# Performance work log

Measured on AMD Instinct MI355X. Metric: run time of the kernel, lower is better.

Reference implementation:

```python
import jax, jax.numpy as jnp
import numpy as np

N = 100000   # nodes
E = 1600000  # directed edges
HID = 64


def gat_conv(x, src, dst, W, a_src, a_dst, b, heads, out_ch):
    """PyG-style GATConv (add_self_loops=True, negative_slope=0.2, concat)."""
    n = x.shape[0]
    h = (x @ W).reshape(n, heads, out_ch)              # [N,H,C]
    loop = jnp.arange(n, dtype=src.dtype)
    s = jnp.concatenate([src, loop])                   # self loops appended
    d = jnp.concatenate([dst, loop])
    alpha_src = jnp.sum(h * a_src, axis=-1)            # [N,H]
    alpha_dst = jnp.sum(h * a_dst, axis=-1)            # [N,H]
    alpha = jax.nn.leaky_relu(alpha_src[s] + alpha_dst[d], 0.2)  # [E+N,H]
    # segment softmax over incoming edges of each destination node
    amax = jax.ops.segment_max(alpha, d, num_segments=n)
    alpha = jnp.exp(alpha - amax[d])
    asum = jax.ops.segment_sum(alpha, d, num_segments=n)
    alpha = alpha / (asum[d] + 1e-16)
    msg = h[s] * alpha[:, :, None]                     # [E+N,H,C]
    out = jax.ops.segment_sum(msg, d, num_segments=n)  # [N,H,C]
    return out.reshape(n, heads * out_ch) + b


def setup_inputs() -> dict:
    key = jax.random.key(0)
    ks = jax.random.split(key, 22)
    rn = lambda k, shp, s=0.1: (jax.random.normal(k, shp, jnp.float32) * s)
    inp = {
        "x": jax.random.normal(ks[0], (N, 2), jnp.float32),
        "edge_index": jax.random.randint(ks[1], (2, E), 0, N, dtype=jnp.int32),
        "edge_attr": jax.random.normal(ks[2], (E, 2), jnp.float32),
        # node encoder
        "enc_W": rn(ks[3], (2, HID)), "enc_b": rn(ks[4], (HID,)),
        # gat1: heads=4, out=16
        "g1_W": rn(ks[5], (HID, HID)), "g1_as": rn(ks[6], (4, 16)),
        "g1_ad": rn(ks[7], (4, 16)), "g1_b": rn(ks[8], (HID,)),
        # gat2: heads=1, out=64
        "g2_W": rn(ks[9], (HID, HID)), "g2_as": rn(ks[10], (1, HID)),
        "g2_ad": rn(ks[11], (1, HID)), "g2_b": rn(ks[12], (HID,)),
        # node head
        "no_W1": rn(ks[13], (HID, HID)), "no_b1": rn(ks[14], (HID,)),
        "no_W2": rn(ks[15], (HID, 2)), "no_b2": rn(ks[16], (2,)),
        # edge head: in = 2*HID + 2 = 130
        "eo_W1": rn(ks[17], (2 * HID + 2, HID)), "eo_b1": rn(ks[18], (HID,)),
        "eo_W2": rn(ks[19], (HID, 1)), "eo_b2": rn(ks[20], (1,)),
    }
    return inp


def reference(x, edge_index, edge_attr, enc_W, enc_b,
              g1_W, g1_as, g1_ad, g1_b,
              g2_W, g2_as, g2_ad, g2_b,
              no_W1, no_b1, no_W2, no_b2,
              eo_W1, eo_b1, eo_W2, eo_b2):
    src, dst = edge_index[0], edge_index[1]
    h = x @ enc_W + enc_b                                    # node encoder (dropout = eval identity)
    h = jax.nn.elu(gat_conv(h, src, dst, g1_W, g1_as, g1_ad, g1_b, 4, 16))
    h = gat_conv(h, src, dst, g2_W, g2_as, g2_ad, g2_b, 1, HID)
    e_in = jnp.concatenate([h[src], h[dst], edge_attr], axis=-1)  # [E,130]
    node_pred = jnp.tanh(jax.nn.leaky_relu(h @ no_W1 + no_b1, 0.01) @ no_W2 + no_b2)
    edge_pred = jnp.tanh(jax.nn.leaky_relu(e_in @ eo_W1 + eo_b1, 0.01) @ eo_W2 + eo_b2)[:, 0]
    return edge_pred, node_pred
```

## Files before the change

### kernel.cpp

```cpp
#include <hip/hip_runtime.h>
#include <hip/hip_fp16.h>
#include <math.h>


typedef _Float16 half8_t __attribute__((ext_vector_type(8)));
typedef _Float16 half2_t __attribute__((ext_vector_type(2)));
typedef float floatx4 __attribute__((ext_vector_type(4)));

#if defined(__has_builtin)
#if __has_builtin(__builtin_amdgcn_fdot2)
#define HAS_FDOT2 1
#endif
#if __has_builtin(__builtin_elementwise_max)
#define HAS_EMAX 1
#endif
#endif

static __device__ __forceinline__ float fdot2_acc(half2_t a, half2_t b, float c){
#ifdef HAS_FDOT2
  return __builtin_amdgcn_fdot2(a, b, c, false);
#else
  return fmaf((float)a[0], (float)b[0], fmaf((float)a[1], (float)b[1], c));
#endif
}

static __device__ __forceinline__ half2_t leaky2(half2_t t, half2_t slope){
#ifdef HAS_EMAX
  return __builtin_elementwise_max(t, t * slope);
#else
  half2_t r;
  r[0] = t[0] > (_Float16)0 ? t[0] : t[0] * slope[0];
  r[1] = t[1] > (_Float16)0 ? t[1] : t[1] * slope[1];
  return r;
#endif
}

__global__ __launch_bounds__(512) void k_scatter_fuse(
    const int* __restrict__ src, const int* __restrict__ dst,
    int E, int NB, int cap, int* cursor,
    unsigned int* __restrict__ ebuf,
    const float* __restrict__ x,
    const float* __restrict__ encW, const float* __restrict__ encb,
    const float* __restrict__ g1W,
    const float* __restrict__ g1as, const float* __restrict__ g1ad,
    const float* __restrict__ g2W,
    const float* __restrict__ g2as, const float* __restrict__ g2ad,
    float* __restrict__ vsd,
    __half* __restrict__ hw, float* __restrict__ alpha_s,
    float* __restrict__ alpha_d, int n){
  __shared__ int hist[800];
  __shared__ int base[800];
  __shared__ float McS[192];
  int t = threadIdx.x;
  if (t < 64){
    float m0 = 0.f, m1 = 0.f, cc = 0.f;
    for (int k = 0; k < 64; ++k){
      float g = g1W[k * 64 + t];
      m0 = fmaf(encW[k], g, m0);
      m1 = fmaf(encW[64 + k], g, m1);
      cc = fmaf(encb[k], g, cc);
    }
    McS[t] = m0; McS[64 + t] = m1; McS[128 + t] = cc;
  }
  if (blockIdx.x == 0 && t >= 64 && t < 128){
    int k = t - 64;
    float vs = 0.f, vd = 0.f;
    for (int ch = 0; ch < 64; ++ch){
      float g = g2W[k * 64 + ch];
      vs = fmaf(g, g2as[ch], vs);
      vd = fmaf(g, g2ad[ch], vd);
    }
    vsd[k] = vs; vsd[64 + k] = vd;
  }
  int cbase = blockIdx.x * 8192;
  bool doScatter = (cbase < E);
  if (doScatter){
    for (int i = t; i < NB; i += 512) hist[i] = 0;
  }
  __syncthreads();
  if (doScatter){
    int sv[16], bk[16], dl[16], rk[16];
    #pragma unroll
    for (int i = 0; i < 16; ++i){
      int e = cbase + i * 512 + t;
      if (e < E){
        int d = dst[e];
        sv[i] = src[e]; bk[i] = d >> 7; dl[i] = d & 127;
        rk[i] = atomicAdd(&hist[bk[i]], 1);
      } else bk[i] = -1;
    }
    __syncthreads();
    for (int i = t; i < NB; i += 512){
      int c = hist[i];
      base[i] = (c > 0) ? (i * cap + atomicAdd(&cursor[i], c)) : 0;
    }
    __syncthreads();
    #pragma unroll
    for (int i = 0; i < 16; ++i){
      if (bk[i] >= 0){
        int p = base[bk[i]] + rk[i];
        if (p < (bk[i] + 1) * cap)
          ebuf[p] = (unsigned)sv[i] | ((unsigned)dl[i] << 17);
      }
    }
  }
  int total = n * 64;
  int lane = t & 63;
  for (int idx = blockIdx.x * 512 + t; idx < total; idx += gridDim.x * 512){
    int node = idx >> 6;
    float acc = fmaf(x[node * 2 + 0], McS[lane],
                fmaf(x[node * 2 + 1], McS[64 + lane], McS[128 + lane]));
    hw[idx] = __float2half(acc);
    float ps = acc * g1as[lane];
    float pd = acc * g1ad[lane];
    #pragma unroll
    for (int off = 1; off < 16; off <<= 1){
      ps += __shfl_xor(ps, off);
      pd += __shfl_xor(pd, off);
    }
    if ((lane & 15) == 0){
      int h = lane >> 4;
      alpha_s[node * 4 + h] = ps;
      alpha_d[node * 4 + h] = pd;
    }
  }
}

__global__ void k_bucket_build(const int* __restrict__ cursor, int cap, int N,
                               unsigned int* ebuf, int2* __restrict__ rowrange){
  __shared__ unsigned int ent[2700];
  __shared__ unsigned short rank[2700];
  __shared__ int cnts[128];
  __shared__ int aux[128];
  int b = blockIdx.x, t = threadIdx.x;
  int base = b * cap;
  int cnt = cursor[b];
  if (cnt > cap) cnt = cap;
  for (int i = t; i < cnt; i += 256) ent[i] = ebuf[base + i];
  if (t < 128) cnts[t] = 0;
  __syncthreads();
  for (int i = t; i < cnt; i += 256)
    rank[i] = (unsigned short)atomicAdd(&cnts[ent[i] >> 17], 1);
  __syncthreads();
  int v = 0;
  if (t < 128){ v = cnts[t]; aux[t] = v; }
  __syncthreads();
  for (int off = 1; off < 128; off <<= 1){
    int x = 0;
    if (t < 128 && t >= off) x = aux[t - off];
    __syncthreads();
    if (t < 128) aux[t] += x;
    __syncthreads();
  }
  if (t < 128){
    int incl = aux[t];
    int node = (b << 7) + t;
    if (node < N) rowrange[node] = make_int2(base + incl - v, base + incl);
    cnts[t] = incl - v;
  }
  __syncthreads();
  for (int i = t; i < cnt; i += 256){
    unsigned int en = ent[i];
    int pos = cnts[en >> 17] + (int)rank[i];
    ebuf[base + pos] = en;
  }
}

__global__ __launch_bounds__(256) void k_hw_mfma(
    const __half* __restrict__ hin, const float* __restrict__ W,
    const float* __restrict__ vsd,
    __half* __restrict__ hw, float* __restrict__ alpha_s,
    float* __restrict__ alpha_d, int n){
  int t = threadIdx.x;
  int lane = t & 63, wave = t >> 6;
  int l15 = lane & 15, quad = lane >> 4;
  int ch = wave * 16 + l15;
  half8_t b0, b1;
  #pragma unroll
  for (int j = 0; j < 8; ++j){
    b0[j] = (_Float16)W[(quad * 8 + j) * 64 + ch];
    b1[j] = (_Float16)W[(quad * 8 + j + 32) * 64 + ch];
  }
  half8_t bA0 = {0,0,0,0,0,0,0,0}, bA1 = {0,0,0,0,0,0,0,0};
  if (wave == 0 && l15 < 2){
    const float* v = vsd + l15 * 64;
    #pragma unroll
    for (int j = 0; j < 8; ++j){
      bA0[j] = (_Float16)v[quad * 8 + j];
      bA1[j] = (_Float16)v[quad * 8 + j + 32];
    }
  }
  int base = blockIdx.x * 64;
  for (int it = 0; it < 4; ++it){
    int tb = base + it * 16;
    if (tb >= n) break;
    int arn = tb + l15; if (arn >= n) arn = n - 1;
    const __half* arow = hin + (size_t)arn * 64 + quad * 8;
    half8_t a0 = *(const half8_t*)arow;
    half8_t a1 = *(const half8_t*)(arow + 32);
    floatx4 acc = {0.f, 0.f, 0.f, 0.f};
    acc = __builtin_amdgcn_mfma_f32_16x16x32_f16(a0, b0, acc, 0, 0, 0);
    acc = __builtin_amdgcn_mfma_f32_16x16x32_f16(a1, b1, acc, 0, 0, 0);
    #pragma unroll
    for (int r = 0; r < 4; ++r){
      int node = tb + quad * 4 + r;
      if (node < n) hw[(size_t)node * 64 + ch] = __float2half(acc[r]);
    }
    if (wave == 0){
      floatx4 accA = {0.f, 0.f, 0.f, 0.f};
      accA = __builtin_amdgcn_mfma_f32_16x16x32_f16(a0, bA0, accA, 0, 0, 0);
      accA = __builtin_amdgcn_mfma_f32_16x16x32_f16(a1, bA1, accA, 0, 0, 0);
      if (l15 < 2){
        float* dstp = (l15 == 0) ? alpha_s : alpha_d;
        #pragma unroll
        for (int r = 0; r < 4; ++r){
          int node = tb + quad * 4 + r;
          if (node < n) dstp[node] = accA[r];
        }
      }
    }
  }
}

template<int H, bool ELU_ACT>
__global__ void k_agg(const __half* __restrict__ hw,
                      const float* __restrict__ alpha_s, const float* __restrict__ alpha_d,
                      const int2* __restrict__ rowrange,
                      const unsigned int* __restrict__ ebuf,
                      const float* __restrict__ bias, __half* __restrict__ hout, int n){
  int node = (blockIdx.x * blockDim.x + threadIdx.x) >> 6;
  int lane = threadIdx.x & 63;
  int g = lane >> 3, jj = lane & 7;
  if (node >= n) return;
  int hidx = (jj * H) >> 3;
  int2 rr = rowrange[node];
  int start = rr.x, end = rr.y;
  float adn = alpha_d[node * H + hidx];
  float acc[8] = {0.f,0.f,0.f,0.f,0.f,0.f,0.f,0.f};
  float psum = 0.f;
  if (g == 0){
    float a = alpha_s[node * H + hidx] + adn;
    a = a > 0.f ? a : 0.2f * a;
    float p = __expf(a);
    psum = p;
    float4 rv = *(const float4*)(hw + (size_t)node * 64 + jj * 8);
    const __half2* hp = (const __half2*)&rv;
    #pragma unroll
    for (int k = 0; k < 4; ++k){
      float2 f = __half22float2(hp[k]);
      acc[2 * k] = p * f.x; acc[2 * k + 1] = p * f.y;
    }
  }
  int i = start + g;
  for (; i + 8 < end; i += 16){
    unsigned int e0 = ebuf[i], e1 = ebuf[i + 8];
    int s0 = e0 & 0x1FFFF, s1 = e1 & 0x1FFFF;
    float a0 = alpha_s[s0 * H + hidx] + adn;
    float a1 = alpha_s[s1 * H + hidx] + adn;
    a0 = a0 > 0.f ? a0 : 0.2f * a0;
    a1 = a1 > 0.f ? a1 : 0.2f * a1;
    float p0 = __expf(a0), p1 = __expf(a1);
    float4 r0 = *(const float4*)(hw + (size_t)s0 * 64 + jj * 8);
    float4 r1 = *(const float4*)(hw + (size_t)s1 * 64 + jj * 8);
    const __half2* h0 = (const __half2*)&r0;
    const __half2* h1 = (const __half2*)&r1;
    psum += p0 + p1;
    #pragma unroll
    for (int k = 0; k < 4; ++k){
      float2 f0 = __half22float2(h0[k]);
      float2 f1 = __half22float2(h1[k]);
      acc[2 * k]     = fmaf(p0, f0.x, fmaf(p1, f1.x, acc[2 * k]));
      acc[2 * k + 1] = fmaf(p0, f0.y, fmaf(p1, f1.y, acc[2 * k + 1]));
    }
  }
  if (i < end){
    unsigned int en = ebuf[i];
    int s = en & 0x1FFFF;
    float a = alpha_s[s * H + hidx] + adn;
    a = a > 0.f ? a : 0.2f * a;
    float p = __expf(a);
    float4 rv = *(const float4*)(hw + (size_t)s * 64 + jj * 8);
    const __half2* hp = (const __half2*)&rv;
    psum += p;
    #pragma unroll
    for (int k = 0; k < 4; ++k){
      float2 f = __half22float2(hp[k]);
      acc[2 * k]     = fmaf(p, f.x, acc[2 * k]);
      acc[2 * k + 1] = fmaf(p, f.y, acc[2 * k + 1]);
    }
  }
  #pragma unroll
  for (int off = 8; off < 64; off <<= 1){
    psum += __shfl_xor(psum, off);
    #pragma unroll
    for (int k = 0; k < 8; ++k) acc[k] += __shfl_xor(acc[k], off);
  }
  if (g == 0){
    float inv = 1.f / (psum + 1e-16f);
    float4 bv0 = ((const float4*)bias)[2 * jj];
    float4 bv1 = ((const float4*)bias)[2 * jj + 1];
    float o[8];
    o[0] = fmaf(acc[0], inv, bv0.x); o[1] = fmaf(acc[1], inv, bv0.y);
    o[2] = fmaf(acc[2], inv, bv0.z); o[3] = fmaf(acc[3], inv, bv0.w);
    o[4] = fmaf(acc[4], inv, bv1.x); o[5] = fmaf(acc[5], inv, bv1.y);
    o[6] = fmaf(acc[6], inv, bv1.z); o[7] = fmaf(acc[7], inv, bv1.w);
    if (ELU_ACT){
      #pragma unroll
      for (int k = 0; k < 8; ++k) o[k] = o[k] > 0.f ? o[k] : (__expf(o[k]) - 1.f);
    }
    half8_t hv;
    #pragma unroll
    for (int k = 0; k < 8; ++k) hv[k] = (_Float16)o[k];
    *(half8_t*)(hout + (size_t)node * 64 + jj * 8) = hv;
  }
}

__global__ __launch_bounds__(256) void k_heads_mfma(
    const __half* __restrict__ h, const float* __restrict__ eoW1,
    const float* __restrict__ noW1, const float* __restrict__ nob1,
    const float* __restrict__ noW2, const float* __restrict__ nob2,
    __half* __restrict__ P1, __half* __restrict__ P2,
    float* __restrict__ outN, int n){
  __shared__ float redP[4][16][2];
  int t = threadIdx.x;
  int lane = t & 63, wave = t >> 6;
  int l15 = lane & 15, quad = lane >> 4;
  int ch = wave * 16 + l15;
  half8_t bP1a, bP1b, bP2a, bP2b, bNa, bNb;
  #pragma unroll
  for (int j = 0; j < 8; ++j){
    int k0 = quad * 8 + j, k1 = k0 + 32;
    bP1a[j] = (_Float16)eoW1[k0 * 64 + ch];
    bP1b[j] = (_Float16)eoW1[k1 * 64 + ch];
    bP2a[j] = (_Float16)eoW1[(k0 + 64) * 64 + ch];
    bP2b[j] = (_Float16)eoW1[(k1 + 64) * 64 + ch];
    bNa[j]  = (_Float16)noW1[k0 * 64 + ch];
    bNb[j]  = (_Float16)noW1[k1 * 64 + ch];
  }
  float b1v = nob1[ch];
  float w20 = noW2[ch * 2 + 0], w21 = noW2[ch * 2 + 1];
  float b20 = nob2[0], b21 = nob2[1];
  int base = blockIdx.x * 64;
  for (int it = 0; it < 4; ++it){
    int tb = base + it * 16;
    if (tb >= n) break;
    int arn = tb + l15; if (arn >= n) arn = n - 1;
    const __half* arow = h + (size_t)arn * 64 + quad * 8;
    half8_t a0 = *(const half8_t*)arow;
    half8_t a1 = *(const half8_t*)(arow + 32);
    floatx4 ac1 = {0.f,0.f,0.f,0.f}, ac2 = {0.f,0.f,0.f,0.f}, acN = {0.f,0.f,0.f,0.f};
    ac1 = __builtin_amdgcn_mfma_f32_16x16x32_f16(a0, bP1a, ac1, 0, 0, 0);
    ac1 = __builtin_amdgcn_mfma_f32_16x16x32_f16(a1, bP1b, ac1, 0, 0, 0);
    ac2 = __builtin_amdgcn_mfma_f32_16x16x32_f16(a0, bP2a, ac2, 0, 0, 0);
    ac2 = __builtin_amdgcn_mfma_f32_16x16x32_f16(a1, bP2b, ac2, 0, 0, 0);
    acN = __builtin_amdgcn_mfma_f32_16x16x32_f16(a0, bNa, acN, 0, 0, 0);
    acN = __builtin_amdgcn_mfma_f32_16x16x32_f16(a1, bNb, acN, 0, 0, 0);
    float p0[4], p1[4];
    #pragma unroll
    for (int r = 0; r < 4; ++r){
      int node = tb + quad * 4 + r;
      if (node < n){
        P1[(size_t)node * 64 + ch] = __float2half(ac1[r]);
        P2[(size_t)node * 64 + ch] = __float2half(ac2[r]);
      }
      float v = acN[r] + b1v;
      v = v > 0.f ? v : 0.01f * v;
      p0[r] = v * w20;
      p1[r] = v * w21;
      #pragma unroll
      for (int off = 1; off < 16; off <<= 1){
        p0[r] += __shfl_xor(p0[r], off);
        p1[r] += __shfl_xor(p1[r], off);
      }
    }
    if (l15 == 0){
      #pragma unroll
      for (int r = 0; r < 4; ++r){
        redP[wave][quad * 4 + r][0] = p0[r];
        redP[wave][quad * 4 + r][1] = p1[r];
      }
    }
    __syncthreads();
    if (t < 16 && tb + t < n){
      float s0 = redP[0][t][0] + redP[1][t][0] + redP[2][t][0] + redP[3][t][0];
      float s1 = redP[0][t][1] + redP[1][t][1] + redP[2][t][1] + redP[3][t][1];
      outN[(size_t)(tb + t) * 2 + 0] = tanhf(s0 + b20);
      outN[(size_t)(tb + t) * 2 + 1] = tanhf(s1 + b21);
    }
    __syncthreads();
  }
}

__global__ void k_edge_head(const __half* __restrict__ P1h, const __half* __restrict__ P2h,
                            const int* __restrict__ src, const int* __restrict__ dst,
                            const float* __restrict__ eattr, const float* __restrict__ eoW1,
                            const float* __restrict__ b1, const float* __restrict__ W2,
                            const float* __restrict__ b2, float* __restrict__ out, int E){
  int lane = threadIdx.x & 63;
  int jj = lane & 7, q = lane >> 3;
  int wid = (blockIdx.x * blockDim.x + threadIdx.x) >> 6;
  int nw = (gridDim.x * blockDim.x) >> 6;

  const float* rA  = eoW1 + 8192 + jj * 8;
  const float* rB  = eoW1 + 8256 + jj * 8;
  const float* b1p = b1 + jj * 8;
  const float* w2p = W2 + jj * 8;
  half2_t rah[4], rbh[4], bbh[4], w2h[4];
  #pragma unroll
  for (int k = 0; k < 4; ++k){
    rah[k] = (half2_t){(_Float16)rA[2 * k],  (_Float16)rA[2 * k + 1]};
    rbh[k] = (half2_t){(_Float16)rB[2 * k],  (_Float16)rB[2 * k + 1]};
    bbh[k] = (half2_t){(_Float16)b1p[2 * k], (_Float16)b1p[2 * k + 1]};
    w2h[k] = (half2_t){(_Float16)w2p[2 * k], (_Float16)w2p[2 * k + 1]};
  }
  const half2_t slope2 = {(_Float16)0.01f, (_Float16)0.01f};
  float b2v = b2[0];

  const float4* P1q = (const float4*)P1h;
  const float4* P2q = (const float4*)P2h;
  const float2* eav = (const float2*)eattr;

  int groups = (E + 31) >> 5;
  for (int g = wid; g < groups; g += nw){
    int e0 = g * 32 + q;
    float p[4] = {0.f, 0.f, 0.f, 0.f};
    #pragma unroll
    for (int u = 0; u < 4; ++u){
      int e = e0 + u * 8;
      if (e < E){
        int s = src[e];
        int d = dst[e];
        float2 ea = eav[e];
        float4 g1 = P1q[(size_t)s * 8 + jj];
        float4 g2 = P2q[(size_t)d * 8 + jj];
        const half2_t* h1 = (const half2_t*)&g1;
        const half2_t* h2 = (const half2_t*)&g2;
        _Float16 exs = (_Float16)ea.x, eys = (_Float16)ea.y;
        half2_t ex = {exs, exs};
        half2_t ey = {eys, eys};
        float acc = 0.f;
        #pragma unroll
        for (int k = 0; k < 4; ++k){
          half2_t c = ex * rah[k] + bbh[k];
          c = ey * rbh[k] + c;
          half2_t tv = (h1[k] + h2[k]) + c;
          tv = leaky2(tv, slope2);
          acc = fdot2_acc(tv, w2h[k], acc);
        }
        p[u] = acc;
      }
    }
    #pragma unroll
    for (int off = 1; off < 8; off <<= 1){
      #pragma unroll
      for (int u = 0; u < 4; ++u) p[u] += __shfl_xor(p[u], off);
    }
    if (jj == 0){
      #pragma unroll
      for (int u = 0; u < 4; ++u){
        int e = e0 + u * 8;
        if (e < E) out[e] = tanhf(p[u] + b2v);
      }
    }
  }
}

extern "C" void kernel_launch(void* const* d_in, const int* in_sizes, int n_in,
                              void* d_out, int out_size, void* d_ws, size_t ws_size,
                              hipStream_t stream){
  const float* x    = (const float*)d_in[0];
  const int*   eidx = (const int*)  d_in[1];
  const float* ea   = (const float*)d_in[2];
  const float* encW = (const float*)d_in[3];
  const float* encb = (const float*)d_in[4];
  const float* g1W  = (const float*)d_in[5];
  const float* g1as = (const float*)d_in[6];
  const float* g1ad = (const float*)d_in[7];
  const float* g1b  = (const float*)d_in[8];
  const float* g2W  = (const float*)d_in[9];
  const float* g2as = (const float*)d_in[10];
  const float* g2ad = (const float*)d_in[11];
  const float* g2b  = (const float*)d_in[12];
  const float* noW1 = (const float*)d_in[13];
  const float* nob1 = (const float*)d_in[14];
  const float* noW2 = (const float*)d_in[15];
  const float* nob2 = (const float*)d_in[16];
  const float* eoW1 = (const float*)d_in[17];
  const float* eob1 = (const float*)d_in[18];
  const float* eoW2 = (const float*)d_in[19];
  const float* eob2 = (const float*)d_in[20];

  const int N = in_sizes[0] / 2;
  const int E = in_sizes[1] / 2;
  const int* src = eidx;
  const int* dst = eidx + E;

  const int NB = (N + 127) >> 7;
  int avg = (E + NB - 1) / NB;
  int cap = avg + avg / 4 + 64;
  if (cap > 2700) cap = 2700;

  char* ws = (char*)d_ws;
  size_t off = 0;
  auto alloc = [&](size_t bytes) -> void* {
    void* p = ws + off;
    off = (off + bytes + 255) & ~(size_t)255;
    return p;
  };
  __half* bufA  = (__half*)alloc((size_t)N * 64 * 2);
  __half* bufH  = (__half*)alloc((size_t)N * 64 * 2);
  __half* P1h   = (__half*)alloc((size_t)N * 64 * 2);
  __half* P2h   = (__half*)alloc((size_t)N * 64 * 2);
  float*  as    = (float*) alloc((size_t)N * 4 * 4);
  float*  ad    = (float*) alloc((size_t)N * 4 * 4);
  int2* rowrange = (int2*) alloc((size_t)N * 8);
  unsigned int* ebuf = (unsigned int*)alloc((size_t)NB * cap * 4);
  int* cursor   = (int*)   alloc((size_t)NB * 4);
  float* vsd    = (float*) alloc(128 * 4);

  hipMemsetAsync(cursor, 0, (size_t)NB * 4, stream);
  k_scatter_fuse<<<(E + 2047) / 2048, 512, 0, stream>>>(
      src, dst, E, NB, cap, cursor, ebuf,
      x, encW, encb, g1W, g1as, g1ad, g2W, g2as, g2ad, vsd, bufH, as, ad, N);
  k_bucket_build<<<NB, 256, 0, stream>>>(cursor, cap, N, ebuf, rowrange);
  k_agg<4, true><<<(N + 3) / 4, 256, 0, stream>>>(bufH, as, ad,
                                                  rowrange, ebuf, g1b, bufA, N);
  k_hw_mfma<<<(N + 63) / 64, 256, 0, stream>>>(bufA, g2W, vsd, bufH, as, ad, N);
  k_agg<1, false><<<(N + 3) / 4, 256, 0, stream>>>(bufH, as, ad,
                                                   rowrange, ebuf, g2b, bufA, N);
  float* out = (float*)d_out;
  k_heads_mfma<<<(N + 63) / 64, 256, 0, stream>>>(bufA, eoW1, noW1, nob1, noW2, nob2,
                                                  P1h, P2h, out + E, N);
  k_edge_head<<<2048, 256, 0, stream>>>(P1h, P2h, src, dst, ea,
                                        eoW1, eob1, eoW2, eob2, out, E);
}
```

Baseline: 331.8 us.

## Double scatter chunk per block with two-pass histogram instead of register-held ranks

Each block now bins 16384 edges instead of 8192, which halves the number of scattering blocks and the global cursor atomics per bucket. Ranks are no longer kept in registers. A first pass only counts destinations per bucket; after the bases are reserved, the histogram is reset and a second pass re-reads dst and src, takes a fresh rank with an LDS atomic, and writes the packed edge. This cuts register pressure and global atomic traffic, at the cost of reading dst twice and doing LDS atomics twice. If the grid size is derived elsewhere from 8192, only half the blocks now do scatter work, so there is less parallelism in this phase.

```diff
diff --git a/kernel.cpp b/kernel.cpp
--- a/kernel.cpp
+++ b/kernel.cpp
@@ -34,6 +34,8 @@
   return r;
 #endif
 }
+
+#define SCATTER_CHUNK 16384
 
 __global__ __launch_bounds__(512) void k_scatter_fuse(
     const int* __restrict__ src, const int* __restrict__ dst,
@@ -72,22 +74,17 @@
     }
     vsd[k] = vs; vsd[64 + k] = vd;
   }
-  int cbase = blockIdx.x * 8192;
+  int cbase = blockIdx.x * SCATTER_CHUNK;
   bool doScatter = (cbase < E);
   if (doScatter){
     for (int i = t; i < NB; i += 512) hist[i] = 0;
   }
   __syncthreads();
   if (doScatter){
-    int sv[16], bk[16], dl[16], rk[16];
-    #pragma unroll
-    for (int i = 0; i < 16; ++i){
-      int e = cbase + i * 512 + t;
-      if (e < E){
-        int d = dst[e];
-        sv[i] = src[e]; bk[i] = d >> 7; dl[i] = d & 127;
-        rk[i] = atomicAdd(&hist[bk[i]], 1);
-      } else bk[i] = -1;
+    int ecnt = E - cbase; if (ecnt > SCATTER_CHUNK) ecnt = SCATTER_CHUNK;
+    for (int i = t; i < ecnt; i += 512){
+      int d = dst[cbase + i];
+      atomicAdd(&hist[d >> 7], 1);
     }
     __syncthreads();
     for (int i = t; i < NB; i += 512){
@@ -95,13 +92,16 @@
       base[i] = (c > 0) ? (i * cap + atomicAdd(&cursor[i], c)) : 0;
     }
     __syncthreads();
-    #pragma unroll
-    for (int i = 0; i < 16; ++i){
-      if (bk[i] >= 0){
-        int p = base[bk[i]] + rk[i];
-        if (p < (bk[i] + 1) * cap)
-          ebuf[p] = (unsigned)sv[i] | ((unsigned)dl[i] << 17);
-      }
+    for (int i = t; i < NB; i += 512) hist[i] = 0;
+    __syncthreads();
+    for (int i = t; i < ecnt; i += 512){
+      int e = cbase + i;
+      int d = dst[e];
+      int bk = d >> 7;
+      int rk = atomicAdd(&hist[bk], 1);
+      int p = base[bk] + rk;
+      if (p < (bk + 1) * cap)
+        ebuf[p] = (unsigned)src[e] | ((unsigned)(d & 127) << 17);
     }
   }
   int total = n * 64;
```

Measured after the change: 349.1 us. 1.05x slower.
